# Kernel tuning notes

Measured on AMD Instinct MI355X. Metric: run time of the kernel, lower is better.

## Reference

```python
import jax, jax.numpy as jnp
import numpy as np

Z, K, H, Y = 128, 256, 512, 4  # z_size, key_size, hidden_size, y_dim


def setup_inputs() -> dict:
    key = jax.random.key(0)
    ks = jax.random.split(key, 8)
    B, T, P = 512, 32, 32
    s = lambda k, shape, sc: (jax.random.normal(k, shape, jnp.float32) * sc)
    return {
        "x_seq": jax.random.normal(ks[0], (B, T, P, P), jnp.float32),
        "W_enc": s(ks[1], (P * P, Z), 0.03),
        "gamma": jnp.ones((Z,), jnp.float32),
        "beta": jnp.zeros((Z,), jnp.float32),
        "W_ih": s(ks[2], (4 * H, K + 1), 0.05),
        "W_hh": s(ks[3], (4 * H, H), 0.04),
        "b_ih": jnp.zeros((4 * H,), jnp.float32),
        "b_hh": jnp.zeros((4 * H,), jnp.float32),
        "W_key": s(ks[4], (K, H), 0.06),
        "b_key": jnp.zeros((K,), jnp.float32),
        "W_g": s(ks[5], (1, H), 0.06),
        "b_g": jnp.zeros((1,), jnp.float32),
        "conf_gain": jnp.ones((1,), jnp.float32),
        "conf_bias": jnp.zeros((1,), jnp.float32),
        "W_y": s(ks[6], (Y, H), 0.06),
        "b_y": jnp.zeros((Y,), jnp.float32),
    }


def _lstm_cell(x, h, c, W_ih, W_hh, b_ih, b_hh):
    # PyTorch gate order: i, f, g, o
    gates = x @ W_ih.T + b_ih + h @ W_hh.T + b_hh
    i, f, g, o = jnp.split(gates, 4, axis=-1)
    c = jax.nn.sigmoid(f) * c + jax.nn.sigmoid(i) * jnp.tanh(g)
    h = jax.nn.sigmoid(o) * jnp.tanh(c)
    return h, c


def _forward(x_seq, W_enc, gamma, beta, W_ih, W_hh, b_ih, b_hh,
             W_key, b_key, W_g, b_g, conf_gain, conf_bias, W_y, b_y):
    B, T, P, _ = x_seq.shape
    # encoder: flatten -> linear to z_size (stand-in for Encoder_mlp)
    z = x_seq.reshape(B, T, P * P) @ W_enc  # [B, T, Z]
    # context norm over the sequence dim (single task segment)
    mu = z.mean(axis=1, keepdims=True)
    sig = jnp.sqrt(z.var(axis=1, keepdims=True) + 1e-8)
    z = (z - mu) / sig * gamma + beta

    M = T + 1  # T+1 steps; final step feeds a zero z_t
    z_pad = jnp.concatenate([z, jnp.zeros((B, 1, Z), z.dtype)], axis=1)  # [B, M, Z]

    h0 = jnp.zeros((B, H), z.dtype)
    c0 = jnp.zeros((B, H), z.dtype)
    kr0 = jnp.zeros((B, K + 1), z.dtype)
    Mk0 = jnp.zeros((B, M, K), z.dtype)
    Mv0 = jnp.zeros((B, M, Z), z.dtype)

    def step(carry, t):
        h, c, key_r, M_k, M_v = carry
        z_t = jax.lax.dynamic_index_in_dim(z_pad, t, axis=1, keepdims=False)  # [B, Z]
        h, c = _lstm_cell(key_r, h, c, W_ih, W_hh, b_ih, b_hh)
        key_w = jax.nn.relu(h @ W_key.T + b_key)          # [B, K]
        g = jax.nn.sigmoid(h @ W_g.T + b_g)               # [B, 1]
        y_lin = h @ W_y.T + b_y                            # [B, Y]
        # attention read over valid memory slots j < t
        scores = jnp.einsum('bz,bmz->bm', z_t, M_v)        # [B, M]
        valid = (jnp.arange(M) < t)[None, :]
        w_k = jax.nn.softmax(jnp.where(valid, scores, -1e9), axis=1)
        c_k = jax.nn.sigmoid(scores * conf_gain + conf_bias)
        kv = jnp.concatenate([M_k, c_k[..., None]], axis=2)  # [B, M, K+1]
        attn = g * jnp.einsum('bm,bmd->bd', w_k, kv)          # [B, K+1]
        key_r_new = jnp.where(t == 0, jnp.zeros_like(attn), attn)
        # append to memory at slot t
        M_k = jax.lax.dynamic_update_slice_in_dim(M_k, key_w[:, None, :], t, axis=1)
        M_v = jax.lax.dynamic_update_slice_in_dim(M_v, z_t[:, None, :], t, axis=1)
        return (h, c, key_r_new, M_k, M_v), y_lin

    _, ys = jax.lax.scan(step, (h0, c0, kr0, Mk0, Mv0), jnp.arange(M))
    return ys[-1]  # y_pred_linear from final step, [B, Y]


def reference(x_seq, W_enc, gamma, beta, W_ih, W_hh, b_ih, b_hh,
              W_key, b_key, W_g, b_g, conf_gain, conf_bias, W_y, b_y):
    y_pred_linear = _forward(x_seq, W_enc, gamma, beta, W_ih, W_hh, b_ih, b_hh,
                             W_key, b_key, W_g, b_g, conf_gain, conf_bias, W_y, b_y)
    y_pred = jnp.argmax(y_pred_linear, axis=1)
    return y_pred_linear, y_pred
```

## Files before the change

### kernel.cpp

```cpp
#include <hip/hip_runtime.h>
#include <math.h>

typedef unsigned short ushort;
typedef unsigned int uint;
typedef __bf16 bf16x8 __attribute__((ext_vector_type(8)));
typedef float f32x4 __attribute__((ext_vector_type(4)));

#define ZS    128
#define KS    256
#define HS    512
#define BATCH 512
#define TT    32
#define MM    33
#define NB    2304
#define KPAD  800
#define HOFF  272
#define LDA   800

static __device__ __forceinline__ float sigf(float x) { return 1.f / (1.f + expf(-x)); }

__global__ void prep_w(const float* __restrict__ W_ih, const float* __restrict__ W_hh,
                       const float* __restrict__ W_key, const float* __restrict__ b_ih,
                       const float* __restrict__ b_hh, const float* __restrict__ b_key,
                       const float* __restrict__ W_enc,
                       ushort* __restrict__ Whi, ushort* __restrict__ Wlo,
                       ushort* __restrict__ Behi, ushort* __restrict__ Belo,
                       float* __restrict__ biasN)
{
    int idx = blockIdx.x * 256 + threadIdx.x;
    if (idx < NB) {
        float bv;
        if (idx < 2048) { int j = idx >> 2, gi = idx & 3, r = gi * 512 + j; bv = b_ih[r] + b_hh[r]; }
        else bv = b_key[idx - 2048];
        biasN[idx] = bv;
    }
    if (idx < NB * KPAD) {
        int n = idx / KPAD, k = idx - n * KPAD;
        float v = 0.f;
        if (n < 2048) {
            int j = n >> 2, gi = n & 3, r = gi * 512 + j;
            if (k < 257) v = W_ih[r * 257 + k];
            else if (k >= HOFF && k < HOFF + 512) v = W_hh[r * 512 + (k - HOFF)];
        } else {
            if (k >= HOFF && k < HOFF + 512) v = W_key[(n - 2048) * 512 + (k - HOFF)];
        }
        uint u = __float_as_uint(v);
        Whi[idx] = (ushort)(u >> 16);
        float lo = v - __uint_as_float(u & 0xFFFF0000u);
        Wlo[idx] = (ushort)(__float_as_uint(lo) >> 16);
    } else if (idx < NB * KPAD + 128 * 1024) {
        int e = idx - NB * KPAD;
        int n = e >> 10, k = e & 1023;
        float v = W_enc[k * 128 + n];
        uint u = __float_as_uint(v);
        Behi[e] = (ushort)(u >> 16);
        float lo = v - __uint_as_float(u & 0xFFFF0000u);
        Belo[e] = (ushort)(__float_as_uint(lo) >> 16);
    }
}

template<int BN, int MODE>
__global__ __launch_bounds__(256)
void gemm_mfma(const float* __restrict__ A, int lda,
               const ushort* __restrict__ Bhi, const ushort* __restrict__ Blo, int ldb,
               int nslice,
               float* __restrict__ out, const float* __restrict__ biasN,
               float* __restrict__ cst, float* __restrict__ Mk, int step)
{
    constexpr int NI = BN / 32;
    constexpr int AHI = 0, ALO = 2560, BHI = 5120, BLO = 5120 + 40 * BN;
    __shared__ ushort lds[5120 + 80 * BN];

    const int tid = threadIdx.x;
    const int bx = blockIdx.x, by = blockIdx.y;
    const int row0 = by * 64, n0 = bx * BN;
    const int l = tid & 63, w = tid >> 6, wm = w >> 1, wn = w & 1;
    const int lm = l & 15, kg = (l >> 4) << 3;

    f32x4 acc[2][NI];
    const f32x4 zero4 = {0.f, 0.f, 0.f, 0.f};
#pragma unroll
    for (int mi = 0; mi < 2; mi++)
#pragma unroll
        for (int ni = 0; ni < NI; ni++) acc[mi][ni] = zero4;

    for (int s = 0; s < nslice; s++) {
        const int k0 = s * 32;
        float4 av[2];
#pragma unroll
        for (int i = 0; i < 2; i++) {
            int idx = tid + 256 * i, r = idx >> 3, c = (idx & 7) << 2;
            av[i] = *(const float4*)(A + (size_t)(row0 + r) * lda + k0 + c);
        }
        uint4 bhv[BN / 64], blv[BN / 64];
#pragma unroll
        for (int i = 0; i < BN / 64; i++) {
            int idx = tid + 256 * i, r = idx >> 2, c = (idx & 3) << 3;
            bhv[i] = *(const uint4*)(Bhi + (size_t)(n0 + r) * ldb + k0 + c);
            blv[i] = *(const uint4*)(Blo + (size_t)(n0 + r) * ldb + k0 + c);
        }
        __syncthreads();
#pragma unroll
        for (int i = 0; i < 2; i++) {
            int idx = tid + 256 * i, r = idx >> 3, c = (idx & 7) << 2;
            uint u0 = __float_as_uint(av[i].x), u1 = __float_as_uint(av[i].y);
            uint u2 = __float_as_uint(av[i].z), u3 = __float_as_uint(av[i].w);
            uint hp0 = (u1 & 0xFFFF0000u) | (u0 >> 16);
            uint hp1 = (u3 & 0xFFFF0000u) | (u2 >> 16);
            float l0 = av[i].x - __uint_as_float(u0 & 0xFFFF0000u);
            float l1 = av[i].y - __uint_as_float(u1 & 0xFFFF0000u);
            float l2 = av[i].z - __uint_as_float(u2 & 0xFFFF0000u);
            float l3 = av[i].w - __uint_as_float(u3 & 0xFFFF0000u);
            uint lp0 = (__float_as_uint(l1) & 0xFFFF0000u) | (__float_as_uint(l0) >> 16);
            uint lp1 = (__float_as_uint(l3) & 0xFFFF0000u) | (__float_as_uint(l2) >> 16);
            *(uint2*)&lds[AHI + r * 40 + c] = make_uint2(hp0, hp1);
            *(uint2*)&lds[ALO + r * 40 + c] = make_uint2(lp0, lp1);
        }
#pragma unroll
        for (int i = 0; i < BN / 64; i++) {
            int idx = tid + 256 * i, r = idx >> 2, c = (idx & 3) << 3;
            *(uint4*)&lds[BHI + r * 40 + c] = bhv[i];
            *(uint4*)&lds[BLO + r * 40 + c] = blv[i];
        }
        __syncthreads();
        bf16x8 ah[2], alv[2], bh[NI], bl[NI];
#pragma unroll
        for (int mi = 0; mi < 2; mi++) {
            int r = wm * 32 + mi * 16 + lm;
            ah[mi]  = *(const bf16x8*)&lds[AHI + r * 40 + kg];
            alv[mi] = *(const bf16x8*)&lds[ALO + r * 40 + kg];
        }
#pragma unroll
        for (int ni = 0; ni < NI; ni++) {
            int r = wn * (BN / 2) + ni * 16 + lm;
            bh[ni] = *(const bf16x8*)&lds[BHI + r * 40 + kg];
            bl[ni] = *(const bf16x8*)&lds[BLO + r * 40 + kg];
        }
#pragma unroll
        for (int mi = 0; mi < 2; mi++)
#pragma unroll
            for (int ni = 0; ni < NI; ni++) {
                acc[mi][ni] = __builtin_amdgcn_mfma_f32_16x16x32_bf16(ah[mi],  bh[ni], acc[mi][ni], 0, 0, 0);
                acc[mi][ni] = __builtin_amdgcn_mfma_f32_16x16x32_bf16(ah[mi],  bl[ni], acc[mi][ni], 0, 0, 0);
                acc[mi][ni] = __builtin_amdgcn_mfma_f32_16x16x32_bf16(alv[mi], bh[ni], acc[mi][ni], 0, 0, 0);
            }
    }

    const int crow = (l >> 4) << 2;
    if (MODE == 0) {
#pragma unroll
        for (int mi = 0; mi < 2; mi++)
#pragma unroll
            for (int ni = 0; ni < NI; ni++)
#pragma unroll
                for (int r = 0; r < 4; r++) {
                    int m = row0 + wm * 32 + mi * 16 + crow + r;
                    int z = n0 + wn * (BN / 2) + ni * 16 + lm;
                    out[(size_t)(m >> 5) * (MM * ZS) + (m & 31) * ZS + z] = acc[mi][ni][r];
                }
    } else if (bx < 32) {
        __syncthreads();
        float* epi = (float*)lds;
        float* ew = epi + w * 1088;
#pragma unroll
        for (int mi = 0; mi < 2; mi++)
#pragma unroll
            for (int ni = 0; ni < NI; ni++)
#pragma unroll
                for (int r = 0; r < 4; r++) {
                    int ml = mi * 16 + crow + r, nl = ni * 16 + lm;
                    ew[ml * 34 + nl] = acc[mi][ni][r] + biasN[n0 + wn * 32 + nl];
                }
        __syncthreads();
        int bl_ = tid >> 2, ug = tid & 3;
        int b = row0 + bl_;
        int j0 = bx * 16 + ug * 4;
        float4 cold = *(float4*)&cst[(size_t)b * HS + j0];
        float cc[4] = {cold.x, cold.y, cold.z, cold.w};
        float hv[4];
#pragma unroll
        for (int i = 0; i < 4; i++) {
            int ul = ug * 4 + i;
            float p[4];
#pragma unroll
            for (int g = 0; g < 4; g++) {
                int nb = ul * 4 + g;
                p[g] = epi[((bl_ >> 5) * 2 + (nb >> 5)) * 1088 + (bl_ & 31) * 34 + (nb & 31)];
            }
            float ig = sigf(p[0]), fg = sigf(p[1]), gg = tanhf(p[2]), og = sigf(p[3]);
            float cn = fg * cc[i] + ig * gg;
            hv[i] = og * tanhf(cn);
            cc[i] = cn;
        }
        *(float4*)&cst[(size_t)b * HS + j0] = make_float4(cc[0], cc[1], cc[2], cc[3]);
        *(float4*)&out[(size_t)b * LDA + HOFF + j0] = make_float4(hv[0], hv[1], hv[2], hv[3]);
    } else if (step >= 1) {
#pragma unroll
        for (int mi = 0; mi < 2; mi++)
#pragma unroll
            for (int ni = 0; ni < NI; ni++)
#pragma unroll
                for (int r = 0; r < 4; r++) {
                    int b = row0 + wm * 32 + mi * 16 + crow + r;
                    int cg = n0 + wn * 32 + ni * 16 + lm;
                    float v = fmaxf(acc[mi][ni][r] + biasN[cg], 0.f);
                    Mk[((size_t)(step - 1) * BATCH + b) * KS + (cg - 2048)] = v;
                }
    }
}

__global__ void norm_k(float* __restrict__ z_pad, const float* __restrict__ gamma,
                       const float* __restrict__ beta)
{
    int b = blockIdx.x, zc = threadIdx.x;
    float* zb = z_pad + (size_t)b * (MM * ZS);
    float s = 0.f, s2 = 0.f;
    for (int t = 0; t < TT; t++) { float v = zb[t * ZS + zc]; s += v; s2 += v * v; }
    float mu = s * (1.f / 32.f);
    float var = s2 * (1.f / 32.f) - mu * mu;
    float rstd = 1.f / sqrtf(var + 1e-8f);
    float ga = gamma[zc], be = beta[zc];
    for (int t = 0; t < TT; t++) {
        float v = zb[t * ZS + zc];
        zb[t * ZS + zc] = (v - mu) * rstd * ga + be;
    }
    zb[TT * ZS + zc] = 0.f;
}

__global__ __launch_bounds__(256)
void scores_k(const float* __restrict__ z_pad, const float* __restrict__ cg_p,
              const float* __restrict__ cb_p, float* __restrict__ watt,
              float* __restrict__ wc)
{
    __shared__ float zs[MM * 129];
    int b = blockIdx.x, tid = threadIdx.x;
    const float* zb = z_pad + (size_t)b * (MM * ZS);
    for (int i = tid; i < MM * ZS; i += 256) {
        int m = i >> 7, k = i & 127;
        zs[m * 129 + k] = zb[i];
    }
    __syncthreads();
    float cg = cg_p[0], cb = cb_p[0];
    int wid = tid >> 6, lane = tid & 63;
    for (int t = 1 + wid; t <= 32; t += 4) {
        int m = lane;
        float s = -3.0e38f;
        if (m < t) {
            const float* zt = &zs[t * 129];
            const float* zm = &zs[m * 129];
            float acc = 0.f;
#pragma unroll 8
            for (int k = 0; k < ZS; k++) acc += zt[k] * zm[k];
            s = acc;
        }
        float mx = s;
        for (int off = 1; off < 64; off <<= 1) mx = fmaxf(mx, __shfl_xor(mx, off));
        float e = (m < t) ? expf(s - mx) : 0.f;
        float sum = e;
        for (int off = 1; off < 64; off <<= 1) sum += __shfl_xor(sum, off);
        float w = e / sum;
        if (m < t) watt[(b * MM + t) * MM + m] = w;
        float p = (m < t) ? w * sigf(s * cg + cb) : 0.f;
        for (int off = 1; off < 64; off <<= 1) p += __shfl_xor(p, off);
        if (lane == 0) wc[b * MM + t] = p;
    }
}

__global__ __launch_bounds__(256)
void post_k(float* __restrict__ inpN, const float* __restrict__ W_g,
            const float* __restrict__ b_g, const float* __restrict__ watt,
            const float* __restrict__ wc, const float* __restrict__ Mk, int t)
{
    __shared__ float red[256];
    __shared__ float wts[32];
    __shared__ float gsh;
    int b = blockIdx.x, tid = threadIdx.x;
    float* row = inpN + (size_t)b * LDA;
    float h1 = row[HOFF + tid], h2 = row[HOFF + 256 + tid];
    red[tid] = h1 * W_g[tid] + h2 * W_g[tid + 256];
    if (tid < t) wts[tid] = watt[(b * MM + t) * MM + tid];
    __syncthreads();
    for (int s = 128; s > 0; s >>= 1) {
        if (tid < s) red[tid] += red[tid + s];
        __syncthreads();
    }
    if (tid == 0) gsh = sigf(red[0] + b_g[0]);
    __syncthreads();
    float g = gsh;
    float acc = 0.f;
    for (int m = 0; m < t; m++)
        acc += wts[m] * Mk[((size_t)m * BATCH + b) * KS + tid];
    row[tid] = g * acc;
    if (tid == 0) row[256] = g * wc[b * MM + t];
}

__global__ void y_k(const float* __restrict__ inpN, const float* __restrict__ W_y,
                    const float* __restrict__ b_y, float* __restrict__ out)
{
    int b = blockIdx.x, lane = threadIdx.x;
    const float* h = inpN + (size_t)b * LDA + HOFF;
    float a0 = 0, a1 = 0, a2 = 0, a3 = 0;
    for (int r = 0; r < 8; r++) {
        int k = lane + r * 64;
        float hv = h[k];
        a0 += hv * W_y[k];
        a1 += hv * W_y[512 + k];
        a2 += hv * W_y[1024 + k];
        a3 += hv * W_y[1536 + k];
    }
    for (int off = 32; off > 0; off >>= 1) {
        a0 += __shfl_xor(a0, off);
        a1 += __shfl_xor(a1, off);
        a2 += __shfl_xor(a2, off);
        a3 += __shfl_xor(a3, off);
    }
    if (lane == 0) {
        float y0 = a0 + b_y[0], y1 = a1 + b_y[1], y2 = a2 + b_y[2], y3 = a3 + b_y[3];
        out[b * 4 + 0] = y0; out[b * 4 + 1] = y1; out[b * 4 + 2] = y2; out[b * 4 + 3] = y3;
        int best = 0; float bv = y0;
        if (y1 > bv) { bv = y1; best = 1; }
        if (y2 > bv) { bv = y2; best = 2; }
        if (y3 > bv) { bv = y3; best = 3; }
        out[2048 + b] = (float)best;
    }
}

extern "C" void kernel_launch(void* const* d_in, const int* in_sizes, int n_in,
                              void* d_out, int out_size, void* d_ws, size_t ws_size,
                              hipStream_t stream)
{
    const float* x_seq = (const float*)d_in[0];
    const float* W_enc = (const float*)d_in[1];
    const float* gamma = (const float*)d_in[2];
    const float* beta  = (const float*)d_in[3];
    const float* W_ih  = (const float*)d_in[4];
    const float* W_hh  = (const float*)d_in[5];
    const float* b_ih  = (const float*)d_in[6];
    const float* b_hh  = (const float*)d_in[7];
    const float* W_key = (const float*)d_in[8];
    const float* b_key = (const float*)d_in[9];
    const float* W_g   = (const float*)d_in[10];
    const float* b_g   = (const float*)d_in[11];
    const float* cgain = (const float*)d_in[12];
    const float* cbias = (const float*)d_in[13];
    const float* W_y   = (const float*)d_in[14];
    const float* b_y   = (const float*)d_in[15];

    float* ws    = (float*)d_ws;
    float* z_pad = ws;
    float* watt  = z_pad + 2162688;
    float* wcv   = watt + 557568;
    float* Mk    = wcv + 16896;
    float* inp0  = Mk + 4194304;
    float* inp1  = inp0 + 409600;
    float* cst   = inp1 + 409600;
    float* biasN = cst + 262144;
    ushort* Whi  = (ushort*)(biasN + 2304);
    ushort* Wlo  = Whi + NB * KPAD;
    ushort* Behi = Wlo + NB * KPAD;
    ushort* Belo = Behi + 131072;

    hipMemsetAsync(inp0, 0, (size_t)(409600 * 2 + 262144) * sizeof(float), stream);

    prep_w<<<(NB * KPAD + 131072 + 255) / 256, 256, 0, stream>>>(
        W_ih, W_hh, W_key, b_ih, b_hh, b_key, W_enc, Whi, Wlo, Behi, Belo, biasN);

    gemm_mfma<128, 0><<<dim3(1, 256), 256, 0, stream>>>(
        x_seq, 1024, Behi, Belo, 1024, 32, z_pad, nullptr, nullptr, nullptr, 0);
    norm_k<<<512, 128, 0, stream>>>(z_pad, gamma, beta);
    scores_k<<<512, 256, 0, stream>>>(z_pad, cgain, cbias, watt, wcv);

    for (int t = 0; t <= 32; t++) {
        float* inC = (t & 1) ? inp1 : inp0;
        float* inN = (t & 1) ? inp0 : inp1;
        gemm_mfma<64, 1><<<dim3(36, 8), 256, 0, stream>>>(
            inC, LDA, Whi, Wlo, KPAD, 25, inN, biasN, cst, Mk, t);
        if (t >= 1 && t <= 31)
            post_k<<<512, 256, 0, stream>>>(inN, W_g, b_g, watt, wcv, Mk, t);
    }
    y_k<<<512, 64, 0, stream>>>(inp1, W_y, b_y, (float*)d_out);
}
```

Before: 1.144 ms.

## Double-buffer LDS tiles in split-bf16 MFMA GEMM to overlap loads with compute

```diff
diff --git a/kernel.cpp b/kernel.cpp
--- a/kernel.cpp
+++ b/kernel.cpp
@@ -69,7 +69,8 @@
 {
     constexpr int NI = BN / 32;
     constexpr int AHI = 0, ALO = 2560, BHI = 5120, BLO = 5120 + 40 * BN;
-    __shared__ ushort lds[5120 + 80 * BN];
+    constexpr int BUF = 5120 + 80 * BN;
+    __shared__ ushort lds[2 * BUF];
 
     const int tid = threadIdx.x;
     const int bx = blockIdx.x, by = blockIdx.y;
@@ -84,22 +85,25 @@
 #pragma unroll
         for (int ni = 0; ni < NI; ni++) acc[mi][ni] = zero4;
 
-    for (int s = 0; s < nslice; s++) {
+    float4 av[2];
+    uint4 bhv[BN / 64], blv[BN / 64];
+
+    auto LOADG = [&](int s) {
         const int k0 = s * 32;
-        float4 av[2];
 #pragma unroll
         for (int i = 0; i < 2; i++) {
             int idx = tid + 256 * i, r = idx >> 3, c = (idx & 7) << 2;
             av[i] = *(const float4*)(A + (size_t)(row0 + r) * lda + k0 + c);
         }
-        uint4 bhv[BN / 64], blv[BN / 64];
 #pragma unroll
         for (int i = 0; i < BN / 64; i++) {
             int idx = tid + 256 * i, r = idx >> 2, c = (idx & 3) << 3;
             bhv[i] = *(const uint4*)(Bhi + (size_t)(n0 + r) * ldb + k0 + c);
             blv[i] = *(const uint4*)(Blo + (size_t)(n0 + r) * ldb + k0 + c);
         }
-        __syncthreads();
+    };
+    auto STORE = [&](int buf) {
+        ushort* L = lds + buf * BUF;
 #pragma unroll
         for (int i = 0; i < 2; i++) {
             int idx = tid + 256 * i, r = idx >> 3, c = (idx & 7) << 2;
@@ -113,28 +117,35 @@
             float l3 = av[i].w - __uint_as_float(u3 & 0xFFFF0000u);
             uint lp0 = (__float_as_uint(l1) & 0xFFFF0000u) | (__float_as_uint(l0) >> 16);
             uint lp1 = (__float_as_uint(l3) & 0xFFFF0000u) | (__float_as_uint(l2) >> 16);
-            *(uint2*)&lds[AHI + r * 40 + c] = make_uint2(hp0, hp1);
-            *(uint2*)&lds[ALO + r * 40 + c] = make_uint2(lp0, lp1);
+            *(uint2*)&L[AHI + r * 40 + c] = make_uint2(hp0, hp1);
+            *(uint2*)&L[ALO + r * 40 + c] = make_uint2(lp0, lp1);
         }
 #pragma unroll
         for (int i = 0; i < BN / 64; i++) {
             int idx = tid + 256 * i, r = idx >> 2, c = (idx & 3) << 3;
-            *(uint4*)&lds[BHI + r * 40 + c] = bhv[i];
-            *(uint4*)&lds[BLO + r * 40 + c] = blv[i];
-        }
+            *(uint4*)&L[BHI + r * 40 + c] = bhv[i];
+            *(uint4*)&L[BLO + r * 40 + c] = blv[i];
+        }
+    };
+
+    LOADG(0);
+    STORE(0);
+    for (int s = 0; s < nslice; s++) {
+        if (s + 1 < nslice) LOADG(s + 1);
         __syncthreads();
+        const ushort* L = lds + (s & 1) * BUF;
         bf16x8 ah[2], alv[2], bh[NI], bl[NI];
 #pragma unroll
         for (int mi = 0; mi < 2; mi++) {
             int r = wm * 32 + mi * 16 + lm;
-            ah[mi]  = *(const bf16x8*)&lds[AHI + r * 40 + kg];
-            alv[mi] = *(const bf16x8*)&lds[ALO + r * 40 + kg];
+            ah[mi]  = *(const bf16x8*)&L[AHI + r * 40 + kg];
+            alv[mi] = *(const bf16x8*)&L[ALO + r * 40 + kg];
         }
 #pragma unroll
         for (int ni = 0; ni < NI; ni++) {
             int r = wn * (BN / 2) + ni * 16 + lm;
-            bh[ni] = *(const bf16x8*)&lds[BHI + r * 40 + kg];
-            bl[ni] = *(const bf16x8*)&lds[BLO + r * 40 + kg];
+            bh[ni] = *(const bf16x8*)&L[BHI + r * 40 + kg];
+            bl[ni] = *(const bf16x8*)&L[BLO + r * 40 + kg];
         }
 #pragma unroll
         for (int mi = 0; mi < 2; mi++)
@@ -144,6 +155,7 @@
                 acc[mi][ni] = __builtin_amdgcn_mfma_f32_16x16x32_bf16(ah[mi],  bl[ni], acc[mi][ni], 0, 0, 0);
                 acc[mi][ni] = __builtin_amdgcn_mfma_f32_16x16x32_bf16(alv[mi], bh[ni], acc[mi][ni], 0, 0, 0);
             }
+        if (s + 1 < nslice) STORE((s + 1) & 1);
     }
 
     const int crow = (l >> 4) << 2;
```

After: 1.140 ms. About the same (-0.4%).
